# Kernel optimization log

Measured on AMD Instinct MI355X. Metric: run time of the kernel, lower is better.

The kernel has to match this reference:

```python
import jax, jax.numpy as jnp
import numpy as np

B, L_IN, L_OUT, N, COV, EMB, H = 32, 336, 48, 512, 4, 32, 64
C = 1 + COV
D_IN = EMB + COV


def setup_inputs() -> dict:
    key = jax.random.key(0)
    ks = jax.random.split(key, 16)
    s = 1.0 / np.sqrt(H)

    def rn(k, shape, scale):
        return jax.random.normal(k, shape, jnp.float32) * scale

    return {
        "history_data": jax.random.normal(ks[0], (B, L_IN, N, C), jnp.float32),
        "future_data": jax.random.normal(ks[1], (B, L_OUT, N, C), jnp.float32),
        "emb_W": rn(ks[2], (EMB, 1), 0.5),
        "emb_b": rn(ks[3], (EMB,), 0.1),
        "W_ih0": rn(ks[4], (4 * H, D_IN), s),
        "W_hh0": rn(ks[5], (4 * H, H), s),
        "b_ih0": rn(ks[6], (4 * H,), s),
        "b_hh0": rn(ks[7], (4 * H,), s),
        "W_ih1": rn(ks[8], (4 * H, H), s),
        "W_hh1": rn(ks[9], (4 * H, H), s),
        "b_ih1": rn(ks[10], (4 * H,), s),
        "b_hh1": rn(ks[11], (4 * H,), s),
        "head_W": rn(ks[12], (2, H), s),
        "head_b": rn(ks[13], (2,), 0.1),
        "train": 1,
    }


def _lstm_cell(x_t, h, c, W_ih, W_hh, b_ih, b_hh):
    # gate order i, f, g, o (torch nn.LSTM convention)
    g = x_t @ W_ih.T + b_ih + h @ W_hh.T + b_hh
    i, f, gg, o = jnp.split(g, 4, axis=-1)
    c = jax.nn.sigmoid(f) * c + jax.nn.sigmoid(i) * jnp.tanh(gg)
    h = jax.nn.sigmoid(o) * jnp.tanh(c)
    return h, c


def _deepar_forward(history_data, future_data, emb_W, emb_b,
                    W_ih0, W_hh0, b_ih0, b_hh0,
                    W_ih1, W_hh1, b_ih1, b_hh1,
                    head_W, head_b):
    Bb, L_in, Nn, _ = history_data.shape
    L_out = future_data.shape[1]
    # [B, L_in+L_out, N, .]
    target = jnp.concatenate([history_data[..., 0:1], future_data[..., 0:1]], axis=1)
    covar = jnp.concatenate([history_data[..., 1:], future_data[..., 1:]], axis=1)
    # train=True branch: teacher forcing for t = 1 .. L-1
    prev = target[:, :-1]        # [B, T, N, 1]
    cov_t = covar[:, 1:]         # [B, T, N, COV]
    emb = prev @ emb_W.T + emb_b  # [B, T, N, EMB]
    x = jnp.concatenate([emb, cov_t], axis=-1)      # [B, T, N, EMB+COV]
    T = x.shape[1]
    x = x.transpose(1, 0, 2, 3).reshape(T, Bb * Nn, -1)  # scan over time
    Hh = W_hh0.shape[1]
    z = jnp.zeros((Bb * Nn, Hh), x.dtype)

    def step(carry, x_t):
        h0, c0, h1, c1 = carry
        h0, c0 = _lstm_cell(x_t, h0, c0, W_ih0, W_hh0, b_ih0, b_hh0)
        h1, c1 = _lstm_cell(h0, h1, c1, W_ih1, W_hh1, b_ih1, b_hh1)
        p = jax.nn.relu(h1) @ head_W.T + head_b       # [BN, 2]
        mu = p[:, 0:1]
        sigma = jax.nn.softplus(p[:, 1:2])
        return (h0, c0, h1, c1), jnp.concatenate([mu, sigma], axis=-1)

    _, outs = jax.lax.scan(step, (z, z, z, z), x)     # [T, BN, 2]
    outs = outs.reshape(T, Bb, Nn, 2).transpose(1, 0, 2, 3)  # [B, T, N, 2]
    return outs[:, -L_out:]


def reference(history_data, future_data, emb_W, emb_b,
              W_ih0, W_hh0, b_ih0, b_hh0,
              W_ih1, W_hh1, b_ih1, b_hh1,
              head_W, head_b, train):
    # train is a static Python int (1 = teacher forcing branch implemented here)
    return _deepar_forward(history_data, future_data, emb_W, emb_b,
                           W_ih0, W_hh0, b_ih0, b_hh0,
                           W_ih1, W_hh1, b_ih1, b_hh1,
                           head_W, head_b)
```

## Files before the change

kernel.cpp:

```cpp
#include <hip/hip_runtime.h>


#define N_PHASES 385
#define AST 168

typedef __attribute__((ext_vector_type(8))) short short8;
typedef __attribute__((ext_vector_type(4))) short s16x4;
typedef __attribute__((ext_vector_type(4))) float floatx4;

__device__ __forceinline__ unsigned short f2bf(float f){
  union { float f; unsigned u; } v; v.f = f;
  unsigned u = v.u + 0x7fffu + ((v.u >> 16) & 1u);
  return (unsigned short)(u >> 16);
}
__device__ __forceinline__ unsigned short f2bf_fast(float f){
  union { float f; unsigned u; } v; v.f = f;
  return (unsigned short)((v.u + 0x8000u) >> 16);
}
__device__ __forceinline__ float bf2f(unsigned short b){
  union { unsigned u; float f; } v; v.u = ((unsigned)b) << 16; return v.f;
}
__device__ __forceinline__ float fsig(float x){
  return __builtin_amdgcn_rcpf(1.f + __expf(-x));
}
__device__ __forceinline__ float ftanh(float x){
  return 1.f - 2.f * __builtin_amdgcn_rcpf(1.f + __expf(2.f * x));
}

__global__ __launch_bounds__(256, 2) void deepar_kernel(
    const float* __restrict__ hist, const float* __restrict__ fut,
    const float* __restrict__ embW, const float* __restrict__ embB,
    const float* __restrict__ Wih0, const float* __restrict__ Whh0,
    const float* __restrict__ bih0, const float* __restrict__ bhh0,
    const float* __restrict__ Wih1, const float* __restrict__ Whh1,
    const float* __restrict__ bih1, const float* __restrict__ bhh1,
    const float* __restrict__ headW, const float* __restrict__ headB,
    float* __restrict__ outp)
{
  const int tid  = threadIdx.x;
  const int lane = tid & 63;
  const int wv   = tid >> 6;
  const int l15  = lane & 15;
  const int quad = lane >> 4;
  const int koff = quad * 8;
  const int jt   = wv;
  const int jbase = jt * 16 + quad * 4;

  const int b  = blockIdx.x >> 4;
  const int n0 = (blockIdx.x & 15) * 32;

  __shared__ __align__(16) unsigned short A[32 * AST];
  __shared__ __align__(16) unsigned short W1[64 * 64 * 8];
  __shared__ float HW[128];

  for (int i = tid; i < 32 * AST; i += 256) A[i] = 0;
  if (tid < 128) HW[tid] = headW[tid];
  __syncthreads();
  if (tid < 32){
    A[tid * AST + 133] = 0x3f80;
    A[tid * AST + 134] = 0x3f80;
  }
  const float hb0 = headB[0], hb1 = headB[1];

  short8 bf0[4][3];
  floatx4 bi1v[4];
  #pragma unroll
  for (int g = 0; g < 4; ++g){
    const int rf = g * 64 + jt * 16 + l15;
    float u = 0.f, bb = bih0[rf] + bhh0[rf];
    #pragma unroll
    for (int e = 0; e < 32; ++e){
      float wval = Wih0[rf * 36 + e];
      u  += wval * embW[e];
      bb += wval * embB[e];
    }
    const unsigned short bbq = f2bf(bb);
    const float bbr = bb - bf2f(bbq);
    #pragma unroll
    for (int kf = 0; kf < 2; ++kf)
      #pragma unroll
      for (int j = 0; j < 8; ++j)
        bf0[g][kf][j] = (short)f2bf(Whh0[rf * 64 + kf * 32 + koff + j]);
    #pragma unroll
    for (int j = 0; j < 8; ++j){
      const int kk = koff + j;
      float v = 0.f;
      if (kk == 0) v = u;
      else if (kk >= 1 && kk <= 4) v = Wih0[rf * 36 + 32 + (kk - 1)];
      else if (kk == 6) v = bbr;
      unsigned short q16 = (kk == 5) ? bbq : f2bf(v);
      bf0[g][2][j] = (short)q16;
    }
    #pragma unroll
    for (int q = 0; q < 4; ++q){
      const int re = g * 64 + jt * 16 + quad * 4 + q;
      bi1v[g][q] = bih1[re] + bhh1[re];
    }
    #pragma unroll
    for (int kf = 0; kf < 4; ++kf){
      const float* src = (kf < 2) ? (Wih1 + rf * 64 + kf * 32)
                                  : (Whh1 + rf * 64 + (kf - 2) * 32);
      short8 w;
      #pragma unroll
      for (int j = 0; j < 8; ++j)
        w[j] = (short)f2bf(src[koff + j]);
      *(short8*)&W1[((jt * 16 + g * 4 + kf) * 64 + lane) * 8] = w;
    }
  }

  const bool isPrev = (tid < 32);
  const bool isCov  = (tid >= 64 && tid < 192);
  int ss = 0, cc = 0;
  if (isPrev){ ss = tid; cc = 0; }
  if (isCov) { ss = (tid - 64) >> 2; cc = 1 + ((tid - 64) & 3); }
  const int myN = n0 + ss;

  auto loadSlab = [&](int tt) -> float {
    if (isPrev){
      int l = tt; if (l > 383) l = 383;
      return (l < 336) ? hist[(((size_t)b * 336 + l) * 512 + myN) * 5]
                       : fut [(((size_t)b * 48 + (l - 336)) * 512 + myN) * 5];
    } else if (isCov){
      int l = tt + 1; if (l > 383) l = 383;
      return (l < 336) ? hist[(((size_t)b * 336 + l) * 512 + myN) * 5 + cc]
                       : fut [(((size_t)b * 48 + (l - 336)) * 512 + myN) * 5 + cc];
    }
    return 0.f;
  };

  float rIn = loadSlab(0);
  if (isPrev || isCov) A[ss * AST + 128 + cc] = f2bf(rIn);
  rIn = loadSlab(1);

  float c0s[8], c1s[8];
  #pragma unroll
  for (int i = 0; i < 8; ++i){ c0s[i] = 0.f; c1s[i] = 0.f; }

  __syncthreads();

  for (int p = 0; p < N_PHASES; ++p){
    const bool doL0 = (p <= 382);
    const bool doL1 = (p >= 1 && p <= 383);

    short8 xh0[2][2], xh1[2][2], xin[2];
    #pragma unroll
    for (int mt = 0; mt < 2; ++mt){
      const int rbase = (mt * 16 + l15) * AST;
      xh0[mt][0] = *(const short8*)&A[rbase +  0 + koff];
      xh0[mt][1] = *(const short8*)&A[rbase + 32 + koff];
      xh1[mt][0] = *(const short8*)&A[rbase + 64 + koff];
      xh1[mt][1] = *(const short8*)&A[rbase + 96 + koff];
      xin[mt]    = *(const short8*)&A[rbase + 128 + koff];
    }

    floatx4 acc0[4][2], acc1[4][2];
    #pragma unroll
    for (int g = 0; g < 4; ++g)
      #pragma unroll
      for (int mt = 0; mt < 2; ++mt){
        floatx4 z = {0.f, 0.f, 0.f, 0.f};
        acc0[g][mt] = z;
        acc1[g][mt] = bi1v[g];
      }

    if (doL0){
      #pragma unroll
      for (int mt = 0; mt < 2; ++mt)
        #pragma unroll
        for (int g = 0; g < 4; ++g){
          acc0[g][mt] = __builtin_amdgcn_mfma_f32_16x16x32_bf16(bf0[g][0], xh0[mt][0], acc0[g][mt], 0, 0, 0);
          acc0[g][mt] = __builtin_amdgcn_mfma_f32_16x16x32_bf16(bf0[g][1], xh0[mt][1], acc0[g][mt], 0, 0, 0);
          acc0[g][mt] = __builtin_amdgcn_mfma_f32_16x16x32_bf16(bf0[g][2], xin[mt],   acc0[g][mt], 0, 0, 0);
        }
    }
    if (doL1){
      #pragma unroll
      for (int kf = 0; kf < 4; ++kf){
        const short8 w0 = *(const short8*)&W1[((jt * 16 +  0 + kf) * 64 + lane) * 8];
        const short8 w1 = *(const short8*)&W1[((jt * 16 +  4 + kf) * 64 + lane) * 8];
        const short8 w2 = *(const short8*)&W1[((jt * 16 +  8 + kf) * 64 + lane) * 8];
        const short8 w3 = *(const short8*)&W1[((jt * 16 + 12 + kf) * 64 + lane) * 8];
        #pragma unroll
        for (int mt = 0; mt < 2; ++mt){
          const short8 xf = (kf < 2) ? xh0[mt][kf] : xh1[mt][kf - 2];
          acc1[0][mt] = __builtin_amdgcn_mfma_f32_16x16x32_bf16(w0, xf, acc1[0][mt], 0, 0, 0);
          acc1[1][mt] = __builtin_amdgcn_mfma_f32_16x16x32_bf16(w1, xf, acc1[1][mt], 0, 0, 0);
          acc1[2][mt] = __builtin_amdgcn_mfma_f32_16x16x32_bf16(w2, xf, acc1[2][mt], 0, 0, 0);
          acc1[3][mt] = __builtin_amdgcn_mfma_f32_16x16x32_bf16(w3, xf, acc1[3][mt], 0, 0, 0);
        }
      }
    }

    float hn0[8], hn1[8];
    if (doL0){
      #pragma unroll
      for (int mt = 0; mt < 2; ++mt)
        #pragma unroll
        for (int q = 0; q < 4; ++q){
          const int idx = mt * 4 + q;
          float iv = acc0[0][mt][q], fv = acc0[1][mt][q];
          float gv = acc0[2][mt][q], ov = acc0[3][mt][q];
          float c = fsig(fv) * c0s[idx] + fsig(iv) * ftanh(gv);
          c0s[idx] = c;
          hn0[idx] = fsig(ov) * ftanh(c);
        }
    }
    if (doL1){
      #pragma unroll
      for (int mt = 0; mt < 2; ++mt)
        #pragma unroll
        for (int q = 0; q < 4; ++q){
          const int idx = mt * 4 + q;
          float iv = acc1[0][mt][q], fv = acc1[1][mt][q];
          float gv = acc1[2][mt][q], ov = acc1[3][mt][q];
          float c = fsig(fv) * c1s[idx] + fsig(iv) * ftanh(gv);
          c1s[idx] = c;
          hn1[idx] = fsig(ov) * ftanh(c);
        }
    }

    if (p >= 337){
      const int hs = tid >> 3, outc = (tid >> 2) & 1, part = tid & 3;
      const short8 hv0 = *(const short8*)&A[hs * AST + 64 + part * 16];
      const short8 hv1 = *(const short8*)&A[hs * AST + 64 + part * 16 + 8];
      float pv = 0.f;
      #pragma unroll
      for (int jj = 0; jj < 8; ++jj){
        float a0 = fmaxf(bf2f((unsigned short)hv0[jj]), 0.f);
        float a1 = fmaxf(bf2f((unsigned short)hv1[jj]), 0.f);
        pv += a0 * HW[outc * 64 + part * 16 + jj];
        pv += a1 * HW[outc * 64 + part * 16 + 8 + jj];
      }
      pv += __shfl_xor(pv, 1);
      pv += __shfl_xor(pv, 2);
      if ((tid & 3) == 0){
        float val;
        if (outc == 0) val = pv + hb0;
        else {
          float x = pv + hb1;
          val = fmaxf(x, 0.f) + __logf(1.f + __expf(-fabsf(x)));
        }
        outp[(((size_t)b * 48 + (p - 337)) * 512 + (n0 + hs)) * 2 + outc] = val;
      }
    }

    __syncthreads();

    if (doL0){
      #pragma unroll
      for (int mt = 0; mt < 2; ++mt){
        s16x4 pk;
        #pragma unroll
        for (int q = 0; q < 4; ++q) pk[q] = (short)f2bf_fast(hn0[mt * 4 + q]);
        *(s16x4*)&A[(mt * 16 + l15) * AST + jbase] = pk;
      }
    }
    if (doL1){
      #pragma unroll
      for (int mt = 0; mt < 2; ++mt){
        s16x4 pk;
        #pragma unroll
        for (int q = 0; q < 4; ++q) pk[q] = (short)f2bf_fast(hn1[mt * 4 + q]);
        *(s16x4*)&A[(mt * 16 + l15) * AST + 64 + jbase] = pk;
      }
    }
    if (isPrev || isCov) A[ss * AST + 128 + cc] = f2bf_fast(rIn);
    rIn = loadSlab(p + 2);

    __syncthreads();
  }
}

extern "C" void kernel_launch(void* const* d_in, const int* in_sizes, int n_in,
                              void* d_out, int out_size, void* d_ws, size_t ws_size,
                              hipStream_t stream) {
  (void)in_sizes; (void)n_in; (void)out_size; (void)d_ws; (void)ws_size;
  deepar_kernel<<<dim3(512), dim3(256), 0, stream>>>(
      (const float*)d_in[0],  (const float*)d_in[1],
      (const float*)d_in[2],  (const float*)d_in[3],
      (const float*)d_in[4],  (const float*)d_in[5],
      (const float*)d_in[6],  (const float*)d_in[7],
      (const float*)d_in[8],  (const float*)d_in[9],
      (const float*)d_in[10], (const float*)d_in[11],
      (const float*)d_in[12], (const float*)d_in[13],
      (float*)d_out);
}
```

Measured before the change: 1.455 ms.

## Double-buffer LSTM state and hold layer-1 weights in registers

Before, layer 0 and layer 1 ran on a skewed wavefront schedule within one phase. Now each timestep runs layer 0, then a barrier, then layer 1 on the fresh h0, using ping-pong LDS buffers so h values are written straight into the next buffer without staging copies. The layer-1 weights move from LDS into registers (w1f), which removes the per-phase LDS weight loads but raises register pressure. The head and output indexing are re-timed to match the new schedule. There are now two barriers per timestep, and each layer's MFMA chain is serialised instead of interleaved, which lengthens the critical path.

```diff
diff --git a/kernel.cpp b/kernel.cpp
--- a/kernel.cpp
+++ b/kernel.cpp
@@ -1,8 +1,8 @@
 #include <hip/hip_runtime.h>
 
 
-#define N_PHASES 385
-#define AST 168
+#define AST  168
+#define ABUF (32 * AST)
 
 typedef __attribute__((ext_vector_type(8))) short short8;
 typedef __attribute__((ext_vector_type(4))) short s16x4;
@@ -49,20 +49,22 @@
   const int b  = blockIdx.x >> 4;
   const int n0 = (blockIdx.x & 15) * 32;
 
-  __shared__ __align__(16) unsigned short A[32 * AST];
-  __shared__ __align__(16) unsigned short W1[64 * 64 * 8];
+  __shared__ __align__(16) unsigned short A[2 * ABUF];
   __shared__ float HW[128];
 
-  for (int i = tid; i < 32 * AST; i += 256) A[i] = 0;
+  for (int i = tid; i < 2 * ABUF; i += 256) A[i] = 0;
   if (tid < 128) HW[tid] = headW[tid];
   __syncthreads();
   if (tid < 32){
-    A[tid * AST + 133] = 0x3f80;
-    A[tid * AST + 134] = 0x3f80;
+    A[tid * AST + 133]        = 0x3f80;
+    A[tid * AST + 134]        = 0x3f80;
+    A[ABUF + tid * AST + 133] = 0x3f80;
+    A[ABUF + tid * AST + 134] = 0x3f80;
   }
   const float hb0 = headB[0], hb1 = headB[1];
 
   short8 bf0[4][3];
+  short8 w1f[4][4];
   floatx4 bi1v[4];
   #pragma unroll
   for (int g = 0; g < 4; ++g){
@@ -92,19 +94,17 @@
       bf0[g][2][j] = (short)q16;
     }
     #pragma unroll
+    for (int kf = 0; kf < 4; ++kf){
+      const float* src = (kf < 2) ? (Wih1 + rf * 64 + kf * 32)
+                                  : (Whh1 + rf * 64 + (kf - 2) * 32);
+      #pragma unroll
+      for (int j = 0; j < 8; ++j)
+        w1f[g][kf][j] = (short)f2bf(src[koff + j]);
+    }
+    #pragma unroll
     for (int q = 0; q < 4; ++q){
       const int re = g * 64 + jt * 16 + quad * 4 + q;
       bi1v[g][q] = bih1[re] + bhh1[re];
-    }
-    #pragma unroll
-    for (int kf = 0; kf < 4; ++kf){
-      const float* src = (kf < 2) ? (Wih1 + rf * 64 + kf * 32)
-                                  : (Whh1 + rf * 64 + (kf - 2) * 32);
-      short8 w;
-      #pragma unroll
-      for (int j = 0; j < 8; ++j)
-        w[j] = (short)f2bf(src[koff + j]);
-      *(short8*)&W1[((jt * 16 + g * 4 + kf) * 64 + lane) * 8] = w;
     }
   }
 
@@ -114,6 +114,7 @@
   if (isPrev){ ss = tid; cc = 0; }
   if (isCov) { ss = (tid - 64) >> 2; cc = 1 + ((tid - 64) & 3); }
   const int myN = n0 + ss;
+  const int sb  = ss * AST + 128 + cc;
 
   auto loadSlab = [&](int tt) -> float {
     if (isPrev){
@@ -129,146 +130,144 @@
   };
 
   float rIn = loadSlab(0);
-  if (isPrev || isCov) A[ss * AST + 128 + cc] = f2bf(rIn);
+  if (isPrev || isCov) A[sb] = f2bf(rIn);
   rIn = loadSlab(1);
 
   float c0s[8], c1s[8];
   #pragma unroll
   for (int i = 0; i < 8; ++i){ c0s[i] = 0.f; c1s[i] = 0.f; }
 
+  const int r0 = l15 * AST;
+  const int r1 = r0 + 16 * AST;
+  const int hd_hs   = tid >> 3;
+  const int hd_outc = (tid >> 2) & 1;
+  const int hd_part = tid & 3;
+  const int hd_base = hd_hs * AST + 64 + hd_part * 16;
+
   __syncthreads();
 
-  for (int p = 0; p < N_PHASES; ++p){
-    const bool doL0 = (p <= 382);
-    const bool doL1 = (p >= 1 && p <= 383);
-
-    short8 xh0[2][2], xh1[2][2], xin[2];
-    #pragma unroll
-    for (int mt = 0; mt < 2; ++mt){
-      const int rbase = (mt * 16 + l15) * AST;
-      xh0[mt][0] = *(const short8*)&A[rbase +  0 + koff];
-      xh0[mt][1] = *(const short8*)&A[rbase + 32 + koff];
-      xh1[mt][0] = *(const short8*)&A[rbase + 64 + koff];
-      xh1[mt][1] = *(const short8*)&A[rbase + 96 + koff];
-      xin[mt]    = *(const short8*)&A[rbase + 128 + koff];
-    }
-
-    floatx4 acc0[4][2], acc1[4][2];
-    #pragma unroll
-    for (int g = 0; g < 4; ++g)
+  auto headOp = [&](int tt, int co){
+    const short8 hv0 = *(const short8*)&A[co + hd_base];
+    const short8 hv1 = *(const short8*)&A[co + hd_base + 8];
+    float pv = 0.f;
+    #pragma unroll
+    for (int jj = 0; jj < 8; ++jj){
+      float a0 = fmaxf(bf2f((unsigned short)hv0[jj]), 0.f);
+      float a1 = fmaxf(bf2f((unsigned short)hv1[jj]), 0.f);
+      pv += a0 * HW[hd_outc * 64 + hd_part * 16 + jj];
+      pv += a1 * HW[hd_outc * 64 + hd_part * 16 + 8 + jj];
+    }
+    pv += __shfl_xor(pv, 1);
+    pv += __shfl_xor(pv, 2);
+    if ((tid & 3) == 0){
+      float val;
+      if (hd_outc == 0) val = pv + hb0;
+      else {
+        float x = pv + hb1;
+        val = fmaxf(x, 0.f) + __logf(1.f + __expf(-fabsf(x)));
+      }
+      outp[(((size_t)b * 48 + (tt - 335)) * 512 + (n0 + hd_hs)) * 2 + hd_outc] = val;
+    }
+  };
+
+  auto phase = [&](int t, int co, int no){
+    {
+      short8 xh[2][2], xin[2];
+      xh[0][0] = *(const short8*)&A[co + r0 + koff];
+      xh[0][1] = *(const short8*)&A[co + r0 + 32 + koff];
+      xin[0]   = *(const short8*)&A[co + r0 + 128 + koff];
+      xh[1][0] = *(const short8*)&A[co + r1 + koff];
+      xh[1][1] = *(const short8*)&A[co + r1 + 32 + koff];
+      xin[1]   = *(const short8*)&A[co + r1 + 128 + koff];
+
+      floatx4 acc[4][2];
+      #pragma unroll
+      for (int g = 0; g < 4; ++g)
+        #pragma unroll
+        for (int mt = 0; mt < 2; ++mt){
+          floatx4 z = {0.f, 0.f, 0.f, 0.f};
+          acc[g][mt] = z;
+        }
+      #pragma unroll
+      for (int mt = 0; mt < 2; ++mt)
+        #pragma unroll
+        for (int g = 0; g < 4; ++g){
+          acc[g][mt] = __builtin_amdgcn_mfma_f32_16x16x32_bf16(bf0[g][0], xh[mt][0], acc[g][mt], 0, 0, 0);
+          acc[g][mt] = __builtin_amdgcn_mfma_f32_16x16x32_bf16(bf0[g][1], xh[mt][1], acc[g][mt], 0, 0, 0);
+          acc[g][mt] = __builtin_amdgcn_mfma_f32_16x16x32_bf16(bf0[g][2], xin[mt],   acc[g][mt], 0, 0, 0);
+        }
       #pragma unroll
       for (int mt = 0; mt < 2; ++mt){
-        floatx4 z = {0.f, 0.f, 0.f, 0.f};
-        acc0[g][mt] = z;
-        acc1[g][mt] = bi1v[g];
-      }
-
-    if (doL0){
-      #pragma unroll
-      for (int mt = 0; mt < 2; ++mt)
-        #pragma unroll
-        for (int g = 0; g < 4; ++g){
-          acc0[g][mt] = __builtin_amdgcn_mfma_f32_16x16x32_bf16(bf0[g][0], xh0[mt][0], acc0[g][mt], 0, 0, 0);
-          acc0[g][mt] = __builtin_amdgcn_mfma_f32_16x16x32_bf16(bf0[g][1], xh0[mt][1], acc0[g][mt], 0, 0, 0);
-          acc0[g][mt] = __builtin_amdgcn_mfma_f32_16x16x32_bf16(bf0[g][2], xin[mt],   acc0[g][mt], 0, 0, 0);
-        }
-    }
-    if (doL1){
-      #pragma unroll
-      for (int kf = 0; kf < 4; ++kf){
-        const short8 w0 = *(const short8*)&W1[((jt * 16 +  0 + kf) * 64 + lane) * 8];
-        const short8 w1 = *(const short8*)&W1[((jt * 16 +  4 + kf) * 64 + lane) * 8];
-        const short8 w2 = *(const short8*)&W1[((jt * 16 +  8 + kf) * 64 + lane) * 8];
-        const short8 w3 = *(const short8*)&W1[((jt * 16 + 12 + kf) * 64 + lane) * 8];
-        #pragma unroll
-        for (int mt = 0; mt < 2; ++mt){
-          const short8 xf = (kf < 2) ? xh0[mt][kf] : xh1[mt][kf - 2];
-          acc1[0][mt] = __builtin_amdgcn_mfma_f32_16x16x32_bf16(w0, xf, acc1[0][mt], 0, 0, 0);
-          acc1[1][mt] = __builtin_amdgcn_mfma_f32_16x16x32_bf16(w1, xf, acc1[1][mt], 0, 0, 0);
-          acc1[2][mt] = __builtin_amdgcn_mfma_f32_16x16x32_bf16(w2, xf, acc1[2][mt], 0, 0, 0);
-          acc1[3][mt] = __builtin_amdgcn_mfma_f32_16x16x32_bf16(w3, xf, acc1[3][mt], 0, 0, 0);
-        }
-      }
-    }
-
-    float hn0[8], hn1[8];
-    if (doL0){
-      #pragma unroll
-      for (int mt = 0; mt < 2; ++mt)
+        s16x4 pk;
         #pragma unroll
         for (int q = 0; q < 4; ++q){
           const int idx = mt * 4 + q;
-          float iv = acc0[0][mt][q], fv = acc0[1][mt][q];
-          float gv = acc0[2][mt][q], ov = acc0[3][mt][q];
+          float iv = acc[0][mt][q], fv = acc[1][mt][q];
+          float gv = acc[2][mt][q], ov = acc[3][mt][q];
           float c = fsig(fv) * c0s[idx] + fsig(iv) * ftanh(gv);
           c0s[idx] = c;
-          hn0[idx] = fsig(ov) * ftanh(c);
-        }
-    }
-    if (doL1){
-      #pragma unroll
-      for (int mt = 0; mt < 2; ++mt)
+          pk[q] = (short)f2bf_fast(fsig(ov) * ftanh(c));
+        }
+        *(s16x4*)&A[no + (mt ? r1 : r0) + jbase] = pk;
+      }
+    }
+    if (isPrev || isCov) A[no + sb] = f2bf_fast(rIn);
+    rIn = loadSlab(t + 2);
+    if (t >= 336) headOp(t - 1, co);
+
+    __syncthreads();
+
+    {
+      short8 y0[2][2], y1[2][2];
+      y0[0][0] = *(const short8*)&A[no + r0 + koff];
+      y0[0][1] = *(const short8*)&A[no + r0 + 32 + koff];
+      y1[0][0] = *(const short8*)&A[co + r0 + 64 + koff];
+      y1[0][1] = *(const short8*)&A[co + r0 + 96 + koff];
+      y0[1][0] = *(const short8*)&A[no + r1 + koff];
+      y0[1][1] = *(const short8*)&A[no + r1 + 32 + koff];
+      y1[1][0] = *(const short8*)&A[co + r1 + 64 + koff];
+      y1[1][1] = *(const short8*)&A[co + r1 + 96 + koff];
+
+      floatx4 acc[4][2];
+      #pragma unroll
+      for (int g = 0; g < 4; ++g)
+        #pragma unroll
+        for (int mt = 0; mt < 2; ++mt)
+          acc[g][mt] = bi1v[g];
+      #pragma unroll
+      for (int kf = 0; kf < 4; ++kf)
+        #pragma unroll
+        for (int mt = 0; mt < 2; ++mt){
+          const short8 xf = (kf < 2) ? y0[mt][kf] : y1[mt][kf - 2];
+          acc[0][mt] = __builtin_amdgcn_mfma_f32_16x16x32_bf16(w1f[0][kf], xf, acc[0][mt], 0, 0, 0);
+          acc[1][mt] = __builtin_amdgcn_mfma_f32_16x16x32_bf16(w1f[1][kf], xf, acc[1][mt], 0, 0, 0);
+          acc[2][mt] = __builtin_amdgcn_mfma_f32_16x16x32_bf16(w1f[2][kf], xf, acc[2][mt], 0, 0, 0);
+          acc[3][mt] = __builtin_amdgcn_mfma_f32_16x16x32_bf16(w1f[3][kf], xf, acc[3][mt], 0, 0, 0);
+        }
+      #pragma unroll
+      for (int mt = 0; mt < 2; ++mt){
+        s16x4 pk;
         #pragma unroll
         for (int q = 0; q < 4; ++q){
           const int idx = mt * 4 + q;
-          float iv = acc1[0][mt][q], fv = acc1[1][mt][q];
-          float gv = acc1[2][mt][q], ov = acc1[3][mt][q];
+          float iv = acc[0][mt][q], fv = acc[1][mt][q];
+          float gv = acc[2][mt][q], ov = acc[3][mt][q];
           float c = fsig(fv) * c1s[idx] + fsig(iv) * ftanh(gv);
           c1s[idx] = c;
-          hn1[idx] = fsig(ov) * ftanh(c);
-        }
-    }
-
-    if (p >= 337){
-      const int hs = tid >> 3, outc = (tid >> 2) & 1, part = tid & 3;
-      const short8 hv0 = *(const short8*)&A[hs * AST + 64 + part * 16];
-      const short8 hv1 = *(const short8*)&A[hs * AST + 64 + part * 16 + 8];
-      float pv = 0.f;
-      #pragma unroll
-      for (int jj = 0; jj < 8; ++jj){
-        float a0 = fmaxf(bf2f((unsigned short)hv0[jj]), 0.f);
-        float a1 = fmaxf(bf2f((unsigned short)hv1[jj]), 0.f);
-        pv += a0 * HW[outc * 64 + part * 16 + jj];
-        pv += a1 * HW[outc * 64 + part * 16 + 8 + jj];
+          pk[q] = (short)f2bf_fast(fsig(ov) * ftanh(c));
+        }
+        *(s16x4*)&A[no + (mt ? r1 : r0) + 64 + jbase] = pk;
       }
-      pv += __shfl_xor(pv, 1);
-      pv += __shfl_xor(pv, 2);
-      if ((tid & 3) == 0){
-        float val;
-        if (outc == 0) val = pv + hb0;
-        else {
-          float x = pv + hb1;
-          val = fmaxf(x, 0.f) + __logf(1.f + __expf(-fabsf(x)));
-        }
-        outp[(((size_t)b * 48 + (p - 337)) * 512 + (n0 + hs)) * 2 + outc] = val;
-      }
-    }
-
+    }
     __syncthreads();
-
-    if (doL0){
-      #pragma unroll
-      for (int mt = 0; mt < 2; ++mt){
-        s16x4 pk;
-        #pragma unroll
-        for (int q = 0; q < 4; ++q) pk[q] = (short)f2bf_fast(hn0[mt * 4 + q]);
-        *(s16x4*)&A[(mt * 16 + l15) * AST + jbase] = pk;
-      }
-    }
-    if (doL1){
-      #pragma unroll
-      for (int mt = 0; mt < 2; ++mt){
-        s16x4 pk;
-        #pragma unroll
-        for (int q = 0; q < 4; ++q) pk[q] = (short)f2bf_fast(hn1[mt * 4 + q]);
-        *(s16x4*)&A[(mt * 16 + l15) * AST + 64 + jbase] = pk;
-      }
-    }
-    if (isPrev || isCov) A[ss * AST + 128 + cc] = f2bf_fast(rIn);
-    rIn = loadSlab(p + 2);
-
-    __syncthreads();
+  };
+
+  for (int tb = 0; tb < 382; tb += 2){
+    phase(tb,     0,    ABUF);
+    phase(tb + 1, ABUF, 0);
   }
+  phase(382, 0, ABUF);
+  headOp(382, ABUF);
 }
 
 extern "C" void kernel_launch(void* const* d_in, const int* in_sizes, int n_in,
```

Result: faster. 1.380 ms (-5.2%).
